# Performance work log

Hardware: AMD Instinct MI355X
Metric: run time of the kernel (lower is better)

The kernel has to match this reference:

```python
import jax, jax.numpy as jnp
import numpy as np


def setup_inputs() -> dict:
    key = jax.random.key(0)
    x = jax.random.normal(key, (8, 48, 48, 48, 64), dtype=jnp.float32)
    gamma = jnp.float32(1e-4)  # matches tf.Variable(0.0001)
    return {"x": x, "gamma": gamma}


def reference(x, gamma):
    # x: (B, W, D, H, C)
    B, W, D, H, C = x.shape
    N = W * D * H
    # Keras Reshape((C, -1)) is a row-major flatten of (W, D, H, C) -> (C, N).
    # NOTE: this is NOT a channels-first transpose; it is a raw reshape,
    # exactly as the original module computes it.
    K = x.reshape(B, C, N)                      # (B, C, N)
    # Q = K^T and J = K^T in the original, so m1 = K@Q and m2 = K@J are both
    # the same Gram matrix G = K @ K^T. Compute it once.
    G = jnp.einsum('bcn,bdn->bcd', K, K)        # (B, C, C)
    m3 = jnp.einsum('bcd,bde->bce', G, G)       # (B, C, C)
    affinity = jax.nn.sigmoid(m3)               # (B, C, C)
    weights = jnp.einsum('bcd,bdn->bcn', affinity, K)  # (B, C, N)
    weights = weights.reshape(B, W, D, H, C)
    return gamma * weights + x
```

## Files before the change

kernel.cpp:

```cpp
#include <hip/hip_runtime.h>

#define NCOL 110592
#define NCH  64
#define CN   (NCOL * NCH)
#define NB   8

typedef __attribute__((ext_vector_type(8))) __bf16 bf16x8;
typedef __attribute__((ext_vector_type(4))) float  f32x4;

__global__ __launch_bounds__(256) void k_gram(const float* __restrict__ x,
                                              float* __restrict__ part,
                                              int steps) {
    const int b     = blockIdx.y;
    const int chunk = blockIdx.x;
    const int tid   = threadIdx.x;
    const int w     = tid >> 6;
    const int lane  = tid & 63;
    const int r     = lane & 15;
    const int q     = lane >> 4;

    const float* xb = x + (size_t)b * CN;

    f32x4 acc0 = {0.f, 0.f, 0.f, 0.f};
    f32x4 acc1 = {0.f, 0.f, 0.f, 0.f};
    f32x4 acc2 = {0.f, 0.f, 0.f, 0.f};
    f32x4 acc3 = {0.f, 0.f, 0.f, 0.f};

    const int kbase = chunk * steps * 32 + q * 8;

    for (int s = 0; s < steps; ++s) {
        const int k0 = kbase + s * 32;
        bf16x8 frag[4];
#pragma unroll
        for (int i = 0; i < 4; ++i) {
            const float* p = xb + (i * 16 + r) * NCOL + k0;
            f32x4 lo = *(const f32x4*)p;
            f32x4 hi = *(const f32x4*)(p + 4);
            bf16x8 f;
            f[0] = (__bf16)lo[0]; f[1] = (__bf16)lo[1];
            f[2] = (__bf16)lo[2]; f[3] = (__bf16)lo[3];
            f[4] = (__bf16)hi[0]; f[5] = (__bf16)hi[1];
            f[6] = (__bf16)hi[2]; f[7] = (__bf16)hi[3];
            frag[i] = f;
        }
        bf16x8 af = (w == 0) ? frag[0] : (w == 1) ? frag[1]
                  : (w == 2) ? frag[2] : frag[3];
        acc0 = __builtin_amdgcn_mfma_f32_16x16x32_bf16(af, frag[0], acc0, 0, 0, 0);
        acc1 = __builtin_amdgcn_mfma_f32_16x16x32_bf16(af, frag[1], acc1, 0, 0, 0);
        acc2 = __builtin_amdgcn_mfma_f32_16x16x32_bf16(af, frag[2], acc2, 0, 0, 0);
        acc3 = __builtin_amdgcn_mfma_f32_16x16x32_bf16(af, frag[3], acc3, 0, 0, 0);
    }

    float* pp = part + (size_t)(b * gridDim.x + chunk) * 4096;
#pragma unroll
    for (int rr = 0; rr < 4; ++rr) {
        const int m = w * 16 + q * 4 + rr;
        pp[m * 64 + (0 * 16 + r)] = acc0[rr];
        pp[m * 64 + (1 * 16 + r)] = acc1[rr];
        pp[m * 64 + (2 * 16 + r)] = acc2[rr];
        pp[m * 64 + (3 * 16 + r)] = acc3[rr];
    }
}

__global__ __launch_bounds__(256) void k_reduce(const float* __restrict__ part,
                                                float* __restrict__ G,
                                                int chunks) {
    const int b    = blockIdx.y;
    const int cell = blockIdx.x * 512 + threadIdx.x;
    float s0 = 0.f, s1 = 0.f;
    for (int p = 0; p < chunks; ++p) {
        const float* pp = part + (size_t)(b * chunks + p) * 4096;
        s0 += pp[cell];
        s1 += pp[cell + 256];
    }
    G[b * 4096 + cell]       = s0;
    G[b * 4096 + cell + 256] = s1;
}

__global__ __launch_bounds__(256) void k_affinity(const float* __restrict__ G,
                                                  const float* __restrict__ gptr,
                                                  float* __restrict__ A) {
    const int b = blockIdx.x;
    __shared__ float Gs[64 * 65];
    const float* Gb = G + b * 4096;
    for (int i = threadIdx.x; i < 4096; i += 256)
        Gs[(i >> 6) * 65 + (i & 63)] = Gb[i];
    __syncthreads();
    const float gamma = gptr[0];
    for (int id = threadIdx.x; id < 4096; id += 256) {
        const int c = id >> 6, e = id & 63;
        float dot = 0.f;
#pragma unroll
        for (int d = 0; d < 64; ++d)
            dot += Gs[c * 65 + d] * Gs[e * 65 + d];
        const float aff = 1.0f / (1.0f + __expf(-dot));
        A[b * 4096 + id] = gamma * aff + ((c == e) ? 1.0f : 0.0f);
    }
}

__global__ __launch_bounds__(256) void k_apply(const float* __restrict__ x,
                                               const float* __restrict__ A,
                                               float* __restrict__ out) {
    const int b  = blockIdx.y;
    const int n0 = blockIdx.x * 512 + threadIdx.x;
    const float* xb = x + (size_t)b * CN;
    float*       ob = out + (size_t)b * CN;
    const float* Ab = A + b * 4096;

    float acc0[64], acc1[64];
#pragma unroll
    for (int c = 0; c < 64; ++c) { acc0[c] = 0.f; acc1[c] = 0.f; }

#pragma unroll 4
    for (int d = 0; d < 64; ++d) {
        const float k0 = xb[d * NCOL + n0];
        const float k1 = xb[d * NCOL + n0 + 256];
#pragma unroll
        for (int c = 0; c < 64; ++c) {
            const float a = Ab[d * 64 + c];
            acc0[c] += a * k0;
            acc1[c] += a * k1;
        }
    }

#pragma unroll
    for (int c = 0; c < 64; ++c) {
        ob[c * NCOL + n0]       = acc0[c];
        ob[c * NCOL + n0 + 256] = acc1[c];
    }
}

extern "C" void kernel_launch(void* const* d_in, const int* in_sizes, int n_in,
                              void* d_out, int out_size, void* d_ws, size_t ws_size,
                              hipStream_t stream) {
    const float* x    = (const float*)d_in[0];
    const float* gptr = (const float*)d_in[1];
    float*       out  = (float*)d_out;
    float*       ws   = (float*)d_ws;

    int chunks = 64;
    auto need = [](int ch) { return (size_t)(8 * ch + 16) * 4096 * 4; };
    if (ws_size < need(64)) chunks = 32;
    if (ws_size < need(32)) chunks = 8;
    if (ws_size < need(8))  chunks = 2;
    const int steps = 3456 / chunks;

    float* part = ws;
    float* G    = ws + (size_t)8 * chunks * 4096;
    float* Aff  = G + 8 * 4096;

    k_gram    <<<dim3(chunks, 8), 256, 0, stream>>>(x, part, steps);
    k_reduce  <<<dim3(8, 8),      256, 0, stream>>>(part, G, chunks);
    k_affinity<<<8,               256, 0, stream>>>(G, gptr, Aff);
    k_apply   <<<dim3(216, 8),    256, 0, stream>>>(x, Aff, out);
}
```

Before: 532.1 us.

## Use bf16 MFMA for apply stage and merge reduce with affinity kernel

The apply stage, previously a scalar FP32 FMA loop with 128 accumulators per thread, now stages 64x64 tiles of K transposed in shared memory and computes A·K with bf16 MFMA. The gamma scale and residual add move into the epilogue, reading the residual from the staged tile. The partial-Gram reduction is folded into the affinity kernel, which removes one launch and the intermediate G buffer. The A·K product is now computed in bf16, which lowers precision but is scaled by a small gamma. The merged post kernel runs on only 8 blocks.

```diff
diff --git a/kernel.cpp b/kernel.cpp
--- a/kernel.cpp
+++ b/kernel.cpp
@@ -1,12 +1,12 @@
 #include <hip/hip_runtime.h>
 
 #define NCOL 110592
-#define NCH  64
-#define CN   (NCOL * NCH)
-#define NB   8
+#define CN   (NCOL * 64)
+#define PAD  66
 
 typedef __attribute__((ext_vector_type(8))) __bf16 bf16x8;
 typedef __attribute__((ext_vector_type(4))) float  f32x4;
+typedef __attribute__((ext_vector_type(2))) float  f32x2;
 
 __global__ __launch_bounds__(256) void k_gram(const float* __restrict__ x,
                                               float* __restrict__ part,
@@ -33,7 +33,7 @@
         bf16x8 frag[4];
 #pragma unroll
         for (int i = 0; i < 4; ++i) {
-            const float* p = xb + (i * 16 + r) * NCOL + k0;
+            const float* p = xb + (size_t)(i * 16 + r) * NCOL + k0;
             f32x4 lo = *(const f32x4*)p;
             f32x4 hi = *(const f32x4*)(p + 4);
             bf16x8 f;
@@ -62,71 +62,106 @@
     }
 }
 
-__global__ __launch_bounds__(256) void k_reduce(const float* __restrict__ part,
-                                                float* __restrict__ G,
-                                                int chunks) {
-    const int b    = blockIdx.y;
-    const int cell = blockIdx.x * 512 + threadIdx.x;
-    float s0 = 0.f, s1 = 0.f;
-    for (int p = 0; p < chunks; ++p) {
-        const float* pp = part + (size_t)(b * chunks + p) * 4096;
-        s0 += pp[cell];
-        s1 += pp[cell + 256];
-    }
-    G[b * 4096 + cell]       = s0;
-    G[b * 4096 + cell + 256] = s1;
-}
-
-__global__ __launch_bounds__(256) void k_affinity(const float* __restrict__ G,
-                                                  const float* __restrict__ gptr,
-                                                  float* __restrict__ A) {
+__global__ __launch_bounds__(256) void k_post(const float* __restrict__ part,
+                                              float* __restrict__ A,
+                                              int chunks) {
     const int b = blockIdx.x;
     __shared__ float Gs[64 * 65];
-    const float* Gb = G + b * 4096;
-    for (int i = threadIdx.x; i < 4096; i += 256)
-        Gs[(i >> 6) * 65 + (i & 63)] = Gb[i];
+    for (int id = threadIdx.x; id < 4096; id += 256) {
+        float s = 0.f;
+        for (int p = 0; p < chunks; ++p)
+            s += part[(size_t)(b * chunks + p) * 4096 + id];
+        Gs[(id >> 6) * 65 + (id & 63)] = s;
+    }
     __syncthreads();
-    const float gamma = gptr[0];
     for (int id = threadIdx.x; id < 4096; id += 256) {
         const int c = id >> 6, e = id & 63;
         float dot = 0.f;
 #pragma unroll
         for (int d = 0; d < 64; ++d)
             dot += Gs[c * 65 + d] * Gs[e * 65 + d];
-        const float aff = 1.0f / (1.0f + __expf(-dot));
-        A[b * 4096 + id] = gamma * aff + ((c == e) ? 1.0f : 0.0f);
+        A[b * 4096 + id] = 1.0f / (1.0f + __expf(-dot));
     }
 }
 
 __global__ __launch_bounds__(256) void k_apply(const float* __restrict__ x,
                                                const float* __restrict__ A,
+                                               const float* __restrict__ gptr,
                                                float* __restrict__ out) {
-    const int b  = blockIdx.y;
-    const int n0 = blockIdx.x * 512 + threadIdx.x;
+    const int b    = blockIdx.y;
+    const int tid  = threadIdx.x;
+    const int w    = tid >> 6;
+    const int lane = tid & 63;
+    const int r    = lane & 15;
+    const int q    = lane >> 4;
+    const float gamma = gptr[0];
+
     const float* xb = x + (size_t)b * CN;
     float*       ob = out + (size_t)b * CN;
     const float* Ab = A + b * 4096;
 
-    float acc0[64], acc1[64];
+    __shared__ float Kt[64 * PAD];
+
+    bf16x8 afr[4][2];
 #pragma unroll
-    for (int c = 0; c < 64; ++c) { acc0[c] = 0.f; acc1[c] = 0.f; }
+    for (int mt = 0; mt < 4; ++mt)
+#pragma unroll
+        for (int ks = 0; ks < 2; ++ks) {
+            const float* p = Ab + (mt * 16 + r) * 64 + ks * 32 + q * 8;
+            f32x4 lo = *(const f32x4*)p;
+            f32x4 hi = *(const f32x4*)(p + 4);
+            bf16x8 f;
+            f[0] = (__bf16)lo[0]; f[1] = (__bf16)lo[1];
+            f[2] = (__bf16)lo[2]; f[3] = (__bf16)lo[3];
+            f[4] = (__bf16)hi[0]; f[5] = (__bf16)hi[1];
+            f[6] = (__bf16)hi[2]; f[7] = (__bf16)hi[3];
+            afr[mt][ks] = f;
+        }
 
-#pragma unroll 4
-    for (int d = 0; d < 64; ++d) {
-        const float k0 = xb[d * NCOL + n0];
-        const float k1 = xb[d * NCOL + n0 + 256];
+    const int nl = w * 16 + r;
+
+    for (int it = 0; it < 8; ++it) {
+        const int n0 = blockIdx.x * 512 + it * 64;
+        __syncthreads();
 #pragma unroll
-        for (int c = 0; c < 64; ++c) {
-            const float a = Ab[d * 64 + c];
-            acc0[c] += a * k0;
-            acc1[c] += a * k1;
+        for (int i = 0; i < 4; ++i) {
+            const int v    = tid + 256 * i;
+            const int row  = v >> 4;
+            const int quad = v & 15;
+            f32x4 vec = *(const f32x4*)(xb + (size_t)row * NCOL + n0 + quad * 4);
+#pragma unroll
+            for (int j = 0; j < 4; ++j)
+                Kt[(quad * 4 + j) * PAD + row] = vec[j];
         }
-    }
+        __syncthreads();
 
+        f32x4 acc[4] = {{0.f,0.f,0.f,0.f},{0.f,0.f,0.f,0.f},
+                        {0.f,0.f,0.f,0.f},{0.f,0.f,0.f,0.f}};
 #pragma unroll
-    for (int c = 0; c < 64; ++c) {
-        ob[c * NCOL + n0]       = acc0[c];
-        ob[c * NCOL + n0 + 256] = acc1[c];
+        for (int ks = 0; ks < 2; ++ks) {
+            const float* kp = &Kt[nl * PAD + ks * 32 + q * 8];
+            f32x2 p0 = *(const f32x2*)(kp + 0);
+            f32x2 p1 = *(const f32x2*)(kp + 2);
+            f32x2 p2 = *(const f32x2*)(kp + 4);
+            f32x2 p3 = *(const f32x2*)(kp + 6);
+            bf16x8 bf;
+            bf[0] = (__bf16)p0[0]; bf[1] = (__bf16)p0[1];
+            bf[2] = (__bf16)p1[0]; bf[3] = (__bf16)p1[1];
+            bf[4] = (__bf16)p2[0]; bf[5] = (__bf16)p2[1];
+            bf[6] = (__bf16)p3[0]; bf[7] = (__bf16)p3[1];
+#pragma unroll
+            for (int mt = 0; mt < 4; ++mt)
+                acc[mt] = __builtin_amdgcn_mfma_f32_16x16x32_bf16(afr[mt][ks], bf, acc[mt], 0, 0, 0);
+        }
+
+        const int n = n0 + nl;
+#pragma unroll
+        for (int mt = 0; mt < 4; ++mt)
+#pragma unroll
+            for (int rr = 0; rr < 4; ++rr) {
+                const int c = mt * 16 + q * 4 + rr;
+                ob[(size_t)c * NCOL + n] = gamma * acc[mt][rr] + Kt[nl * PAD + c];
+            }
     }
 }
 
@@ -139,18 +174,16 @@
     float*       ws   = (float*)d_ws;
 
     int chunks = 64;
-    auto need = [](int ch) { return (size_t)(8 * ch + 16) * 4096 * 4; };
+    auto need = [](int ch) { return (size_t)(8 * ch + 8) * 4096 * 4; };
     if (ws_size < need(64)) chunks = 32;
     if (ws_size < need(32)) chunks = 8;
     if (ws_size < need(8))  chunks = 2;
     const int steps = 3456 / chunks;
 
     float* part = ws;
-    float* G    = ws + (size_t)8 * chunks * 4096;
-    float* Aff  = G + 8 * 4096;
+    float* Aff  = ws + (size_t)8 * chunks * 4096;
 
-    k_gram    <<<dim3(chunks, 8), 256, 0, stream>>>(x, part, steps);
-    k_reduce  <<<dim3(8, 8),      256, 0, stream>>>(part, G, chunks);
-    k_affinity<<<8,               256, 0, stream>>>(G, gptr, Aff);
-    k_apply   <<<dim3(216, 8),    256, 0, stream>>>(x, Aff, out);
+    k_gram <<<dim3(chunks, 8), 256, 0, stream>>>(x, part, steps);
+    k_post <<<8,               256, 0, stream>>>(part, Aff, chunks);
+    k_apply<<<dim3(216, 8),    256, 0, stream>>>(x, Aff, gptr, out);
 }
```

Measured after the change: 724.4 us. 36.1% more time.
